# Kernel tuning notes

Hardware: AMD Instinct MI355X
Metric: run time of the kernel (lower is better)

Reference implementation:

```python
import jax, jax.numpy as jnp
import numpy as np

B, N, C, H, KC, STAGES = 8, 4096, 256, 8, 128, 3
C4 = 4 * C
HD = C4 // H
SCALE = (C // H) ** -0.5  # torch uses head_dim of ORIGINAL dim: (256//8)^-0.5


def _l2norm(x, axis):
    # torch: inp / (1e-6 + inp.norm(dim=axis, keepdim=True))
    return x / (1e-6 + jnp.linalg.norm(x, axis=axis, keepdims=True))


def _dta_branch(xc):
    """EM-style clustering on one stream. xc: [B, 4C, N] -> bases [B, 4C, KC]."""
    b, c, n = xc.shape
    # AdaptiveMaxPool1d(KC): N % KC == 0 -> uniform windows of size N//KC
    bases = _l2norm(xc.reshape(b, c, KC, n // KC).max(axis=-1), axis=1)
    xn = xc.transpose(0, 2, 1)  # [B, N, 4C]
    for _ in range(STAGES):
        z = jax.nn.softmax(jnp.einsum('bnc,bck->bnk', xn, bases), axis=2)  # [B,N,KC]
        z = _l2norm(z, axis=1)
        bases = _l2norm(jnp.einsum('bnc,bnk->bck', xn, z), axis=1)  # [B,4C,KC]
    return bases


def setup_inputs() -> dict:
    key = jax.random.key(0)
    ks = jax.random.split(key, 6)
    x = jax.random.normal(ks[0], (B, N, C), jnp.float32)
    Wq = jax.random.normal(ks[1], (C4, C), jnp.float32) * 0.02
    Wk = jax.random.normal(ks[2], (C4, C), jnp.float32) * 0.02
    Wv = jax.random.normal(ks[3], (C4, C), jnp.float32) * 0.02
    Wp = jax.random.normal(ks[4], (C, C4), jnp.float32) * 0.02
    bp = jnp.zeros((C,), jnp.float32)
    return {"x": x, "Wq": Wq, "Wk": Wk, "Wv": Wv, "Wp": Wp, "bp": bp}


def reference(x, Wq, Wk, Wv, Wp, bp):
    # q/k/v projections (bias-free), [B,N,4C]
    q = x @ Wq.T
    k = x @ Wk.T
    v = x @ Wv.T
    # DTA: note torch does `q, k = self.DA(q, k)` where DA(x1,x2) returns
    # (bases_from_x1, bases_from_x2) -> q bases from q-stream, k bases from k-stream.
    qb = _dta_branch(q.transpose(0, 2, 1))  # [B,4C,KC]
    kb = _dta_branch(k.transpose(0, 2, 1))  # [B,4C,KC]
    qh = qb.reshape(B, H, HD, KC)  # == torch q.permute(0,1,3,2): [B,H,hd,KC]
    kh = kb.reshape(B, H, HD, KC)
    vh = v.transpose(0, 2, 1).reshape(B, H, HD, N)  # [B,H,hd,N]
    # att over cluster axis KC -> [B,H,hd,hd]
    att = jax.nn.softmax(jnp.einsum('bhdk,bhek->bhde', qh, kh) * SCALE, axis=-1)
    o = jnp.einsum('bhde,bhen->bhdn', att, vh)  # [B,H,hd,N]
    # rearrange 'b n_h head_dim n -> b n (n_h head_dim)'
    o = o.transpose(0, 3, 1, 2).reshape(B, N, C4)
    return jax.nn.relu(o @ Wp.T + bp)
```

## Files before the change

kernel.cpp:

```cpp
#include <hip/hip_runtime.h>
#include <hip/hip_bf16.h>

#define NSEQ 4096
#define C4   1024
#define SCALE_F 0.17677669529663687f
#define SLC   524288

typedef __attribute__((ext_vector_type(8))) short bf16x8;
typedef __attribute__((ext_vector_type(4))) float f32x4;
typedef __attribute__((ext_vector_type(8))) unsigned short u16x8;
typedef __attribute__((ext_vector_type(4))) unsigned short u16x4;

__device__ __forceinline__ unsigned short f2b(float x){
  union{float f; unsigned u;} v; v.f = x;
  unsigned r = v.u + 0x7fffu + ((v.u>>16)&1u);
  return (unsigned short)(r>>16);
}
__device__ __forceinline__ unsigned mapf(float x){
  unsigned u = __float_as_uint(x);
  return (u & 0x80000000u) ? ~u : (u | 0x80000000u);
}
__device__ __forceinline__ float unmapf(unsigned m){
  unsigned u = (m & 0x80000000u) ? (m ^ 0x80000000u) : ~m;
  return __uint_as_float(u);
}

typedef __attribute__((address_space(1))) void* gas_p;
typedef __attribute__((address_space(3))) void* las_p;
#define GLDS16(gp, lp) __builtin_amdgcn_global_load_lds((gas_p)(gp), (las_p)(lp), 16, 0, 0)

#define WAITVM8() asm volatile("s_waitcnt vmcnt(8)" ::: "memory")
#define WAITVM4() asm volatile("s_waitcnt vmcnt(4)" ::: "memory")
#define WAITVM0() asm volatile("s_waitcnt vmcnt(0)" ::: "memory")
#define WAITLGKM() asm volatile("s_waitcnt lgkmcnt(0)" ::: "memory")
__device__ __forceinline__ void barrier(){
  asm volatile("" ::: "memory");
  __builtin_amdgcn_s_barrier();
  asm volatile("" ::: "memory");
}

__device__ __forceinline__ void stage128x64s(const unsigned short* G, int row0, int ld, int k0,
                                             unsigned short* lds, int tid){
#pragma unroll
  for (int i = 0; i < 4; ++i){
    int cid = i*256 + tid;
    int r = cid >> 3, c8 = cid & 7;
    GLDS16(G + (row0 + r)*ld + k0 + ((c8 ^ (r & 7))*8), lds + cid*8);
  }
}

template<int LD, int NK, int MA, int MB>
__device__ __forceinline__ void mma_tiles(const unsigned short* ldsA, const unsigned short* ldsB,
                                          f32x4 acc[4][4], int wr, int wc, int lane){
  const int rowg = lane & 15, q4 = lane >> 4;
#pragma unroll
  for (int kc = 0; kc < NK; ++kc){
    bf16x8 a[4], b[4];
#pragma unroll
    for (int mf = 0; mf < 4; ++mf){
      int row = wr*64 + mf*16 + rowg;
      int off;
      if constexpr (MA == 1) off = ((kc*4 + q4) ^ (row & 7)) * 8;
      else                   off = kc*32 + q4*8;
      a[mf] = *(const bf16x8*)(ldsA + row*LD + off);
    }
#pragma unroll
    for (int nf = 0; nf < 4; ++nf){
      int col = wc*64 + nf*16 + rowg;
      int off;
      if constexpr (MB == 1)      off = ((kc*4 + q4) ^ (col & 7)) * 8;
      else if constexpr (MB == 2) off = (kc*32 + q4*8) ^ ((((col>>3) ^ col) & 7) << 3);
      else                        off = kc*32 + q4*8;
      b[nf] = *(const bf16x8*)(ldsB + col*LD + off);
    }
#pragma unroll
    for (int mf = 0; mf < 4; ++mf)
#pragma unroll
      for (int nf = 0; nf < 4; ++nf)
        acc[mf][nf] = __builtin_amdgcn_mfma_f32_16x16x32_bf16(a[mf], b[nf], acc[mf][nf], 0, 0, 0);
  }
}

__global__ __launch_bounds__(256) void k_cast(const float* __restrict__ src,
                                              unsigned short* __restrict__ dst, int n){
  int i = (blockIdx.x*256 + threadIdx.x) * 4;
  if (i < n){
    float4 v = *(const float4*)(src + i);
    u16x4 o = { f2b(v.x), f2b(v.y), f2b(v.z), f2b(v.w) };
    *(u16x4*)(dst + i) = o;
  }
}

__global__ __launch_bounds__(256) void k_transpose_w(const float* __restrict__ src,
                                                     unsigned short* __restrict__ dst,
                                                     int dstLd, int colOff){
  int t = blockIdx.x*256 + threadIdx.x;
  int j = t & 255, r = t >> 8;
  dst[j*dstLd + colOff + r] = f2b(src[r*256 + j]);
}

__global__ __launch_bounds__(256) void k_gemm_qk(const unsigned short* __restrict__ xbf,
                                                 const unsigned short* __restrict__ Wcat,
                                                 unsigned* __restrict__ pooled){
  __shared__ __align__(16) unsigned short ldsA[128*64];
  __shared__ __align__(16) unsigned short ldsB[128*64];
  int tid = threadIdx.x, lane = tid & 63, wid = tid >> 6, wr = wid >> 1, wc = wid & 1;
  int m0 = blockIdx.x*128, n0 = blockIdx.y*128;
  f32x4 acc[4][4] = {};
  for (int k0 = 0; k0 < 256; k0 += 64){
    __syncthreads();
    stage128x64s(xbf,  m0, 256, k0, ldsA, tid);
    stage128x64s(Wcat, n0, 256, k0, ldsB, tid);
    __syncthreads();
    mma_tiles<64,2,1,1>(ldsA, ldsB, acc, wr, wc, lane);
  }
  int colg = lane & 15;
  int b = m0 >> 12, kbase = (m0 & 4095) >> 5;
#pragma unroll
  for (int nf = 0; nf < 4; ++nf){
    float wlo = -3e38f, whi = -3e38f;
#pragma unroll
    for (int r = 0; r < 4; ++r){
      wlo = fmaxf(wlo, fmaxf(acc[0][nf][r], acc[1][nf][r]));
      whi = fmaxf(whi, fmaxf(acc[2][nf][r], acc[3][nf][r]));
    }
    wlo = fmaxf(wlo, __shfl_xor(wlo, 16)); wlo = fmaxf(wlo, __shfl_xor(wlo, 32));
    whi = fmaxf(whi, __shfl_xor(whi, 16)); whi = fmaxf(whi, __shfl_xor(whi, 32));
    if (lane < 16){
      int col = n0 + wc*64 + nf*16 + colg;
      int sbp = b + ((col >> 10) << 3);
      int c4 = col & 1023;
      atomicMax(&pooled[(sbp*128 + kbase + wr*2    )*C4 + c4], mapf(wlo));
      atomicMax(&pooled[(sbp*128 + kbase + wr*2 + 1)*C4 + c4], mapf(whi));
    }
  }
}

__global__ __launch_bounds__(256) void k_norm(const float* __restrict__ bRaw,
                                              const unsigned* __restrict__ pooled,
                                              unsigned short* __restrict__ basesT, int S){
  int row = blockIdx.x, tid = threadIdx.x, lane = tid & 63, wid = tid >> 6;
  float4 v;
  if (S == 0){
    uint4 u = *(const uint4*)(pooled + row*C4 + tid*4);
    v.x = unmapf(u.x); v.y = unmapf(u.y); v.z = unmapf(u.z); v.w = unmapf(u.w);
  } else {
    v = *(const float4*)(bRaw + row*C4 + tid*4);
  }
  float ss = v.x*v.x + v.y*v.y + v.z*v.z + v.w*v.w;
  __shared__ float red[5];
#pragma unroll
  for (int o = 32; o; o >>= 1) ss += __shfl_down(ss, o);
  if (lane == 0) red[wid] = ss;
  __syncthreads();
  if (tid == 0) red[4] = 1.f / (1e-6f + sqrtf(red[0] + red[1] + red[2] + red[3]));
  __syncthreads();
  float inv = red[4];
  u16x4 o4 = { f2b(v.x*inv), f2b(v.y*inv), f2b(v.z*inv), f2b(v.w*inv) };
  *(u16x4*)(basesT + row*C4 + tid*4) = o4;
}

__global__ __launch_bounds__(256) void k_pb(const unsigned short* __restrict__ basesT,
                                            const unsigned short* __restrict__ WcatT,
                                            float* __restrict__ part){
  __shared__ __align__(16) unsigned short ldsA[128*64];
  __shared__ __align__(16) unsigned short ldsB[128*64];
  int tid = threadIdx.x, lane = tid & 63, wid = tid >> 6, wr = wid >> 1, wc = wid & 1;
  int n0 = blockIdx.x*128, sb = blockIdx.y, ks = blockIdx.z;
  const unsigned short* A = basesT + sb*(128*C4);
  int off = (sb >= 8) ? 1024 : 0;
  f32x4 acc[4][4] = {};
  for (int t = 0; t < 4; ++t){
    __syncthreads();
    stage128x64s(A,     0,  C4,   ks*256 + t*64, ldsA, tid);
    stage128x64s(WcatT, n0, 2048, off + ks*256 + t*64, ldsB, tid);
    __syncthreads();
    mma_tiles<64,2,1,1>(ldsA, ldsB, acc, wr, wc, lane);
  }
  int colg = lane & 15, rowg = (lane >> 4) * 4;
#pragma unroll
  for (int mf = 0; mf < 4; ++mf)
#pragma unroll
    for (int nf = 0; nf < 4; ++nf)
#pragma unroll
      for (int r = 0; r < 4; ++r)
        part[ks*SLC + (sb*128 + wr*64 + mf*16 + rowg + r)*256 + n0 + wc*64 + nf*16 + colg]
          = acc[mf][nf][r];
}

__global__ __launch_bounds__(256) void k_redgt(const float* __restrict__ src,
                                               unsigned short* __restrict__ dst, int S){
  int i = (blockIdx.x*256 + threadIdx.x) * 4;
  float4 a = {0.f,0.f,0.f,0.f};
  for (int s = 0; s < S; ++s){
    float4 u = *(const float4*)(src + s*SLC + i);
    a.x += u.x; a.y += u.y; a.z += u.z; a.w += u.w;
  }
  u16x4 o = { f2b(a.x), f2b(a.y), f2b(a.z), f2b(a.w) };
  *(u16x4*)(dst + i) = o;
}

__global__ __launch_bounds__(256) void k_gemm_z(const unsigned short* __restrict__ xbf,
                                                const unsigned short* __restrict__ PBT,
                                                unsigned short* __restrict__ zT){
  __shared__ __align__(16) unsigned short smem[32768];
  __shared__ float redb[2][2][128];
  unsigned short* zt = smem;
  int tid = threadIdx.x, lane = tid & 63, wid = tid >> 6, wr = wid >> 1, wc = wid & 1;
  int m0 = blockIdx.x*128, sb = blockIdx.y;
  const unsigned short* A = xbf + (sb & 7)*(NSEQ*256);
  const unsigned short* B = PBT + sb*(128*256);
  f32x4 acc[4][4] = {};
  stage128x64s(A, m0, 256, 0, smem, tid);
  stage128x64s(B, 0,  256, 0, smem + 16384, tid);
  for (int t = 0; t < 4; ++t){
    int cur = t & 1;
    if (t < 3){
      stage128x64s(A, m0, 256, (t+1)*64, smem + (cur^1)*8192, tid);
      stage128x64s(B, 0,  256, (t+1)*64, smem + 16384 + (cur^1)*8192, tid);
      WAITVM8();
    } else WAITVM0();
    barrier();
    mma_tiles<64,2,1,1>(smem + cur*8192, smem + 16384 + cur*8192, acc, wr, wc, lane);
    WAITLGKM();
    barrier();
  }
  int colg = lane & 15, rowg = (lane >> 4) * 4;
  float sm[4][4];
#pragma unroll
  for (int mf = 0; mf < 4; ++mf)
#pragma unroll
    for (int r = 0; r < 4; ++r){
      float m = fmaxf(fmaxf(acc[mf][0][r], acc[mf][1][r]), fmaxf(acc[mf][2][r], acc[mf][3][r]));
#pragma unroll
      for (int o = 1; o < 16; o <<= 1) m = fmaxf(m, __shfl_xor(m, o));
      if (colg == 0) redb[0][wc][wr*64 + mf*16 + rowg + r] = m;
    }
  barrier();
#pragma unroll
  for (int mf = 0; mf < 4; ++mf)
#pragma unroll
    for (int r = 0; r < 4; ++r){
      int idx = wr*64 + mf*16 + rowg + r;
      float m = fmaxf(redb[0][0][idx], redb[0][1][idx]);
      float s = 0.f;
#pragma unroll
      for (int nf = 0; nf < 4; ++nf){
        float e = __expf(acc[mf][nf][r] - m);
        acc[mf][nf][r] = e; s += e;
      }
#pragma unroll
      for (int o = 1; o < 16; o <<= 1) s += __shfl_xor(s, o);
      if (colg == 0) redb[1][wc][idx] = s;
    }
  barrier();
#pragma unroll
  for (int mf = 0; mf < 4; ++mf)
#pragma unroll
    for (int r = 0; r < 4; ++r){
      int idx = wr*64 + mf*16 + rowg + r;
      sm[mf][r] = 1.f / (redb[1][0][idx] + redb[1][1][idx]);
    }
#pragma unroll
  for (int mf = 0; mf < 4; ++mf)
#pragma unroll
    for (int nf = 0; nf < 4; ++nf){
      int k = wc*64 + nf*16 + colg;
      int swz = (k & 7) << 3;
#pragma unroll
      for (int r = 0; r < 4; ++r){
        int n = wr*64 + mf*16 + rowg + r;
        zt[k*128 + (n ^ swz)] = f2b(acc[mf][nf][r] * sm[mf][r]);
      }
    }
  WAITLGKM();
  barrier();
#pragma unroll
  for (int i = 0; i < 8; ++i){
    int cid = i*256 + tid;
    int kk = cid >> 4, j8 = cid & 15;
    int nbase = (j8*8) ^ ((kk & 7) << 3);
    *(uint4*)(zT + sb*(128*NSEQ) + kk*NSEQ + m0 + nbase) = *(const uint4*)(zt + kk*128 + j8*8);
  }
}

__global__ __launch_bounds__(256) void k_gemm_gt(const unsigned short* __restrict__ xbf,
                                                 const unsigned short* __restrict__ zT,
                                                 float* __restrict__ part){
  __shared__ __align__(16) unsigned short ldsA[2][8192];
  __shared__ __align__(16) unsigned short ldsB[2][8192];
  int tid = threadIdx.x, lane = tid & 63, wid = tid >> 6, wr = wid >> 1, wc = wid & 1;
  int c0 = blockIdx.x*128, sb = blockIdx.y, ks = blockIdx.z;
  const unsigned short* xb = xbf + (sb & 7)*(NSEQ*256);
  const unsigned short* Zt = zT + sb*(128*NSEQ);
  int base = ks*512;
  f32x4 acc[4][4] = {};
  u16x8 vB[4];
  int np_[4], c8_[4];
#pragma unroll
  for (int i = 0; i < 4; ++i){
    int cid = i*256 + tid;
    np_[i] = cid >> 4; c8_[i] = cid & 15;
  }
  stage128x64s(Zt, 0, NSEQ, base, ldsA[0], tid);
#pragma unroll
  for (int i = 0; i < 4; ++i)
    vB[i] = *(const u16x8*)(xb + (base + np_[i])*256 + c0 + c8_[i]*8);
  for (int t = 0; t < 8; ++t){
    int cur = t & 1, n0 = base + t*64;
    if (t < 7){
      stage128x64s(Zt, 0, NSEQ, n0 + 64, ldsA[cur^1], tid);
      WAITVM4();
    } else WAITVM0();
#pragma unroll
    for (int i = 0; i < 4; ++i){
#pragma unroll
      for (int j = 0; j < 8; ++j)
        ldsB[cur][(c8_[i]*8 + j)*64 + (np_[i] ^ (((c8_[i] ^ j) & 7) << 3))] = vB[i][j];
    }
    WAITLGKM();
    barrier();
    if (t < 7){
#pragma unroll
      for (int i = 0; i < 4; ++i)
        vB[i] = *(const u16x8*)(xb + (n0 + 64 + np_[i])*256 + c0 + c8_[i]*8);
    }
    mma_tiles<64,2,1,2>(ldsA[cur], ldsB[cur], acc, wr, wc, lane);
    WAITLGKM();
    barrier();
  }
  int colg = lane & 15, rowg = (lane >> 4) * 4;
#pragma unroll
  for (int mf = 0; mf < 4; ++mf)
#pragma unroll
    for (int nf = 0; nf < 4; ++nf)
#pragma unroll
      for (int r = 0; r < 4; ++r)
        part[ks*SLC + (sb*128 + wr*64 + mf*16 + rowg + r)*256 + c0 + wc*64 + nf*16 + colg]
          = acc[mf][nf][r];
}

__global__ __launch_bounds__(256) void k_pbases(const unsigned short* __restrict__ Wcat,
                                                const unsigned short* __restrict__ GTbf,
                                                float* __restrict__ bRaw){
  __shared__ __align__(16) unsigned short ldsA[128*64];
  __shared__ __align__(16) unsigned short ldsB[128*64];
  int tid = threadIdx.x, lane = tid & 63, wid = tid >> 6, wr = wid >> 1, wc = wid & 1;
  int m0 = blockIdx.x*128, sb = blockIdx.y;
  const unsigned short* A = Wcat + ((sb >= 8) ? 1024*256 : 0);
  const unsigned short* B = GTbf + sb*(128*256);
  f32x4 acc[4][4] = {};
  for (int t = 0; t < 4; ++t){
    __syncthreads();
    stage128x64s(A, m0, 256, t*64, ldsA, tid);
    stage128x64s(B, 0,  256, t*64, ldsB, tid);
    __syncthreads();
    mma_tiles<64,2,1,1>(ldsA, ldsB, acc, wr, wc, lane);
  }
  int colg = lane & 15, rowg = (lane >> 4) * 4;
#pragma unroll
  for (int mf = 0; mf < 4; ++mf)
#pragma unroll
    for (int nf = 0; nf < 4; ++nf)
#pragma unroll
      for (int r = 0; r < 4; ++r){
        int c4 = m0 + wr*64 + mf*16 + rowg + r;
        int k  = wc*64 + nf*16 + colg;
        bRaw[(sb*128 + k)*C4 + c4] = acc[mf][nf][r];
      }
}

__global__ __launch_bounds__(256) void k_attn(const unsigned short* __restrict__ basesT,
                                              unsigned short* __restrict__ attT){
  __shared__ __align__(16) char smem[98816];
  unsigned short* Qlt = (unsigned short*)smem;
  unsigned short* Klt = (unsigned short*)(smem + 32768);
  float* scores       = (float*)smem;
  unsigned short* at  = (unsigned short*)(smem + 66048);
  int tid = threadIdx.x, lane = tid & 63, wid = tid >> 6, wr = wid >> 1, wc = wid & 1;
  int b = blockIdx.x >> 3, h = blockIdx.x & 7;
  const unsigned short* Q = basesT + b*(128*C4) + h*128;
  const unsigned short* K = basesT + (8 + b)*(128*C4) + h*128;
#pragma unroll
  for (int i = 0; i < 8; ++i){
    int cid = i*256 + tid, kk = cid >> 4, c8 = cid & 15;
    u16x8 vq = *(const u16x8*)(Q + kk*C4 + c8*8);
    u16x8 vk = *(const u16x8*)(K + kk*C4 + c8*8);
#pragma unroll
    for (int j = 0; j < 8; ++j){
      Qlt[(c8*8 + j)*128 + kk] = vq[j];
      Klt[(c8*8 + j)*128 + kk] = vk[j];
    }
  }
  __syncthreads();
  f32x4 acc[4][4] = {};
  mma_tiles<128,4,0,0>(Qlt, Klt, acc, wr, wc, lane);
  __syncthreads();
  int colg = lane & 15, rowg = (lane >> 4) * 4;
#pragma unroll
  for (int mf = 0; mf < 4; ++mf)
#pragma unroll
    for (int nf = 0; nf < 4; ++nf)
#pragma unroll
      for (int r = 0; r < 4; ++r)
        scores[(wr*64 + mf*16 + rowg + r)*129 + wc*64 + nf*16 + colg] = acc[mf][nf][r] * SCALE_F;
  __syncthreads();
  if (tid < 128){
    float mx = -3e38f;
    for (int j = 0; j < 128; ++j) mx = fmaxf(mx, scores[tid*129 + j]);
    float s = 0.f;
    for (int j = 0; j < 128; ++j){ float e = __expf(scores[tid*129 + j] - mx); scores[tid*129 + j] = e; s += e; }
    float inv = 1.f / s;
    for (int j = 0; j < 128; ++j) at[j*128 + tid] = f2b(scores[tid*129 + j] * inv);
  }
  __syncthreads();
#pragma unroll
  for (int i = 0; i < 8; ++i){
    int cid = i*256 + tid;
    *(uint4*)(attT + blockIdx.x*16384 + cid*8) = *(const uint4*)(at + cid*8);
  }
}

__global__ __launch_bounds__(256) void k_wpeff(const unsigned short* __restrict__ Wpbf,
                                               const unsigned short* __restrict__ attT,
                                               unsigned short* __restrict__ WpEff){
  __shared__ __align__(16) unsigned short ldsA[128*64];
  __shared__ __align__(16) unsigned short ldsB[128*64];
  int tid = threadIdx.x, lane = tid & 63, wid = tid >> 6, wr = wid >> 1, wc = wid & 1;
  int m0 = blockIdx.x*128;
  int bh = blockIdx.y, b = bh >> 3, h = bh & 7;
  const unsigned short* At = attT + bh*16384;
  f32x4 acc[4][4] = {};
  for (int k0 = 0; k0 < 128; k0 += 64){
    __syncthreads();
    stage128x64s(Wpbf, m0, C4, h*128 + k0, ldsA, tid);
    stage128x64s(At,   0,  128, k0, ldsB, tid);
    __syncthreads();
    mma_tiles<64,2,1,1>(ldsA, ldsB, acc, wr, wc, lane);
  }
  int colg = lane & 15, rowg = (lane >> 4) * 4;
#pragma unroll
  for (int mf = 0; mf < 4; ++mf)
#pragma unroll
    for (int nf = 0; nf < 4; ++nf)
#pragma unroll
      for (int r = 0; r < 4; ++r){
        int row = m0 + wr*64 + mf*16 + rowg + r;
        int col = wc*64 + nf*16 + colg;
        WpEff[b*(256*C4) + row*C4 + h*128 + col] = f2b(acc[mf][nf][r]);
      }
}

__global__ __launch_bounds__(256) void k_gemm_w2(const unsigned short* __restrict__ WpEff,
                                                 const unsigned short* __restrict__ WvT,
                                                 unsigned short* __restrict__ W2){
  __shared__ __align__(16) unsigned short ldsA[128*64];
  __shared__ __align__(16) unsigned short ldsB[128*64];
  int tid = threadIdx.x, lane = tid & 63, wid = tid >> 6, wr = wid >> 1, wc = wid & 1;
  int m0 = blockIdx.x*128, n0 = blockIdx.y*128, b = blockIdx.z;
  const unsigned short* A = WpEff + b*(256*C4);
  f32x4 acc[4][4] = {};
  for (int k0 = 0; k0 < C4; k0 += 64){
    __syncthreads();
    stage128x64s(A,   m0, C4, k0, ldsA, tid);
    stage128x64s(WvT, n0, C4, k0, ldsB, tid);
    __syncthreads();
    mma_tiles<64,2,1,1>(ldsA, ldsB, acc, wr, wc, lane);
  }
  int colg = lane & 15, rowg = (lane >> 4) * 4;
#pragma unroll
  for (int mf = 0; mf < 4; ++mf)
#pragma unroll
    for (int nf = 0; nf < 4; ++nf)
#pragma unroll
      for (int r = 0; r < 4; ++r){
        int row = m0 + wr*64 + mf*16 + rowg + r;
        int col = n0 + wc*64 + nf*16 + colg;
        W2[b*65536 + row*256 + col] = f2b(acc[mf][nf][r]);
      }
}

__global__ __launch_bounds__(256) void k_gemm_out(const unsigned short* __restrict__ xbf,
                                                  const unsigned short* __restrict__ W2,
                                                  const float* __restrict__ bp,
                                                  float* __restrict__ out){
  __shared__ __align__(16) unsigned short ldsA[2][8192];
  __shared__ __align__(16) unsigned short ldsB[2][8192];
  int tid = threadIdx.x, lane = tid & 63, wid = tid >> 6, wr = wid >> 1, wc = wid & 1;
  int m0 = blockIdx.x*128, n0 = blockIdx.y*128, b = blockIdx.z;
  const unsigned short* A = xbf + b*(NSEQ*256);
  const unsigned short* Bm = W2 + b*65536;
  f32x4 acc[4][4] = {};
  stage128x64s(A,  m0, 256, 0, ldsA[0], tid);
  stage128x64s(Bm, n0, 256, 0, ldsB[0], tid);
  for (int t = 0; t < 4; ++t){
    int cur = t & 1;
    if (t < 3){
      stage128x64s(A,  m0, 256, (t+1)*64, ldsA[cur^1], tid);
      stage128x64s(Bm, n0, 256, (t+1)*64, ldsB[cur^1], tid);
      WAITVM8();
    } else WAITVM0();
    barrier();
    mma_tiles<64,2,1,1>(ldsA[cur], ldsB[cur], acc, wr, wc, lane);
    WAITLGKM();
    barrier();
  }
  int colg = lane & 15, rowg = (lane >> 4) * 4;
#pragma unroll
  for (int mf = 0; mf < 4; ++mf)
#pragma unroll
    for (int nf = 0; nf < 4; ++nf){
      int col = n0 + wc*64 + nf*16 + colg;
      float bias = bp[col];
#pragma unroll
      for (int r = 0; r < 4; ++r){
        int row = m0 + wr*64 + mf*16 + rowg + r;
        out[(b*NSEQ + row)*256 + col] = fmaxf(acc[mf][nf][r] + bias, 0.f);
      }
    }
}

extern "C" void kernel_launch(void* const* d_in, const int* in_sizes, int n_in,
                              void* d_out, int out_size, void* d_ws, size_t ws_size,
                              hipStream_t stream){
  (void)in_sizes; (void)n_in; (void)out_size; (void)ws_size;
  const float* x  = (const float*)d_in[0];
  const float* Wq = (const float*)d_in[1];
  const float* Wk = (const float*)d_in[2];
  const float* Wv = (const float*)d_in[3];
  const float* Wp = (const float*)d_in[4];
  const float* bp = (const float*)d_in[5];
  float* out = (float*)d_out;
  char* ws = (char*)d_ws;

  unsigned short* xbf    = (unsigned short*)(ws + 0);
  unsigned short* zT     = (unsigned short*)(ws + 16777216);
  float*          bPart  = (float*)(ws + 50331648);
  float*          bRawP  = (float*)(ws + 67108864);
  unsigned*       pooled = (unsigned*)(ws + 75497472);
  unsigned short* basesT = (unsigned short*)(ws + 83886080);
  unsigned short* PBT    = (unsigned short*)(ws + 88080384);
  unsigned short* GTbf   = (unsigned short*)(ws + 89128960);
  unsigned short* Wcat   = (unsigned short*)(ws + 90177536);
  unsigned short* WcatT  = (unsigned short*)(ws + 91226112);
  unsigned short* WvT    = (unsigned short*)(ws + 92274688);
  unsigned short* Wpbf   = (unsigned short*)(ws + 92798976);
  unsigned short* WpEff  = (unsigned short*)(ws + 93323264);
  unsigned short* attT   = (unsigned short*)(ws + 97517568);
  unsigned short* W2     = (unsigned short*)(ws + 99614720);

  k_cast<<<8192, 256, 0, stream>>>(x,  xbf, 8388608);
  k_cast<<<256,  256, 0, stream>>>(Wq, Wcat,          262144);
  k_cast<<<256,  256, 0, stream>>>(Wk, Wcat + 262144, 262144);
  k_cast<<<256,  256, 0, stream>>>(Wp, Wpbf,          262144);
  k_transpose_w<<<1024, 256, 0, stream>>>(Wv, WvT,   1024, 0);
  k_transpose_w<<<1024, 256, 0, stream>>>(Wq, WcatT, 2048, 0);
  k_transpose_w<<<1024, 256, 0, stream>>>(Wk, WcatT, 2048, 1024);

  (void)hipMemsetAsync(pooled, 0, (size_t)16*128*1024*4, stream);
  k_gemm_qk<<<dim3(256, 16), 256, 0, stream>>>(xbf, Wcat, pooled);
  k_norm<<<2048, 256, 0, stream>>>(bRawP, pooled, basesT, 0);

  for (int st = 0; st < 3; ++st){
    k_pb<<<dim3(2, 16, 4), 256, 0, stream>>>(basesT, WcatT, bPart);
    k_redgt<<<512, 256, 0, stream>>>(bPart, PBT, 4);
    k_gemm_z<<<dim3(32, 16), 256, 0, stream>>>(xbf, PBT, zT);
    k_gemm_gt<<<dim3(2, 16, 8), 256, 0, stream>>>(xbf, zT, bPart);
    k_redgt<<<512, 256, 0, stream>>>(bPart, GTbf, 8);
    k_pbases<<<dim3(8, 16), 256, 0, stream>>>(Wcat, GTbf, bRawP);
    k_norm<<<2048, 256, 0, stream>>>(bRawP, pooled, basesT, 1);
  }

  k_attn<<<64, 256, 0, stream>>>(basesT, attT);
  k_wpeff<<<dim3(2, 64), 256, 0, stream>>>(Wpbf, attT, WpEff);
  k_gemm_w2<<<dim3(2, 2, 8), 256, 0, stream>>>(WpEff, WvT, W2);
  k_gemm_out<<<dim3(32, 2, 8), 256, 0, stream>>>(xbf, W2, bp, out);
}
```

Baseline: 303.3 us.

## Fuse z softmax GEMM with GT accumulation and drop split-K reductions

The z computation is merged with the following G^T = z^T x GEMM, so each block reuses its z tile from LDS, transposes the x tile in LDS and atomically accumulates into an fp32 GT buffer. This removes the zT round trip to global memory and the separate split-K GT kernel and reduce. k_pb now runs the full K loop with double buffering instead of split-K plus a reduce. The weight cast and transpose launches are merged into one kernel. In exchange it adds fp32 atomics, a memset per stage, fewer blocks for k_pb, and a non-deterministic summation order.

```diff
diff --git a/kernel.cpp b/kernel.cpp
--- a/kernel.cpp
+++ b/kernel.cpp
@@ -4,7 +4,6 @@
 #define NSEQ 4096
 #define C4   1024
 #define SCALE_F 0.17677669529663687f
-#define SLC   524288
 
 typedef __attribute__((ext_vector_type(8))) short bf16x8;
 typedef __attribute__((ext_vector_type(4))) float f32x4;
@@ -30,7 +29,6 @@
 #define GLDS16(gp, lp) __builtin_amdgcn_global_load_lds((gas_p)(gp), (las_p)(lp), 16, 0, 0)
 
 #define WAITVM8() asm volatile("s_waitcnt vmcnt(8)" ::: "memory")
-#define WAITVM4() asm volatile("s_waitcnt vmcnt(4)" ::: "memory")
 #define WAITVM0() asm volatile("s_waitcnt vmcnt(0)" ::: "memory")
 #define WAITLGKM() asm volatile("s_waitcnt lgkmcnt(0)" ::: "memory")
 __device__ __forceinline__ void barrier(){
@@ -91,12 +89,31 @@
   }
 }
 
-__global__ __launch_bounds__(256) void k_transpose_w(const float* __restrict__ src,
-                                                     unsigned short* __restrict__ dst,
-                                                     int dstLd, int colOff){
+__global__ __launch_bounds__(256) void k_wprep(const float* __restrict__ Wq, const float* __restrict__ Wk,
+                                               const float* __restrict__ Wv, const float* __restrict__ Wp,
+                                               unsigned short* __restrict__ Wcat,
+                                               unsigned short* __restrict__ Wpbf,
+                                               unsigned short* __restrict__ WcatT,
+                                               unsigned short* __restrict__ WvT){
   int t = blockIdx.x*256 + threadIdx.x;
-  int j = t & 255, r = t >> 8;
-  dst[j*dstLd + colOff + r] = f2b(src[r*256 + j]);
+  int s = blockIdx.y;
+  if (s < 3){
+    const float* src = (s == 0) ? Wq : (s == 1) ? Wk : Wp;
+    unsigned short* dst = (s == 0) ? Wcat : (s == 1) ? (Wcat + 262144) : Wpbf;
+    int i = t*4;
+    float4 v = *(const float4*)(src + i);
+    u16x4 o = { f2b(v.x), f2b(v.y), f2b(v.z), f2b(v.w) };
+    *(u16x4*)(dst + i) = o;
+  } else {
+    const float* src = (s == 3) ? Wv : (s == 4) ? Wq : Wk;
+    unsigned short* dst = (s == 3) ? WvT : WcatT;
+    int ld  = (s == 3) ? 1024 : 2048;
+    int off = (s == 5) ? 1024 : 0;
+    int j = t & 255, r0 = (t >> 8) * 4;
+    u16x4 o = { f2b(src[(r0+0)*256 + j]), f2b(src[(r0+1)*256 + j]),
+                f2b(src[(r0+2)*256 + j]), f2b(src[(r0+3)*256 + j]) };
+    *(u16x4*)(dst + j*ld + off + r0) = o;
+  }
 }
 
 __global__ __launch_bounds__(256) void k_gemm_qk(const unsigned short* __restrict__ xbf,
@@ -162,20 +179,27 @@
 
 __global__ __launch_bounds__(256) void k_pb(const unsigned short* __restrict__ basesT,
                                             const unsigned short* __restrict__ WcatT,
-                                            float* __restrict__ part){
-  __shared__ __align__(16) unsigned short ldsA[128*64];
-  __shared__ __align__(16) unsigned short ldsB[128*64];
-  int tid = threadIdx.x, lane = tid & 63, wid = tid >> 6, wr = wid >> 1, wc = wid & 1;
-  int n0 = blockIdx.x*128, sb = blockIdx.y, ks = blockIdx.z;
+                                            unsigned short* __restrict__ PBT){
+  __shared__ __align__(16) unsigned short ldsA[2][8192];
+  __shared__ __align__(16) unsigned short ldsB[2][8192];
+  int tid = threadIdx.x, lane = tid & 63, wid = tid >> 6, wr = wid >> 1, wc = wid & 1;
+  int n0 = blockIdx.x*128, sb = blockIdx.y;
   const unsigned short* A = basesT + sb*(128*C4);
   int off = (sb >= 8) ? 1024 : 0;
   f32x4 acc[4][4] = {};
-  for (int t = 0; t < 4; ++t){
-    __syncthreads();
-    stage128x64s(A,     0,  C4,   ks*256 + t*64, ldsA, tid);
-    stage128x64s(WcatT, n0, 2048, off + ks*256 + t*64, ldsB, tid);
-    __syncthreads();
-    mma_tiles<64,2,1,1>(ldsA, ldsB, acc, wr, wc, lane);
+  stage128x64s(A,     0,  C4,   0, ldsA[0], tid);
+  stage128x64s(WcatT, n0, 2048, off, ldsB[0], tid);
+  for (int t = 0; t < 16; ++t){
+    int cur = t & 1;
+    if (t < 15){
+      stage128x64s(A,     0,  C4,   (t+1)*64, ldsA[cur^1], tid);
+      stage128x64s(WcatT, n0, 2048, off + (t+1)*64, ldsB[cur^1], tid);
+      WAITVM8();
+    } else WAITVM0();
+    barrier();
+    mma_tiles<64,2,1,1>(ldsA[cur], ldsB[cur], acc, wr, wc, lane);
+    WAITLGKM();
+    barrier();
   }
   int colg = lane & 15, rowg = (lane >> 4) * 4;
 #pragma unroll
@@ -184,28 +208,17 @@
     for (int nf = 0; nf < 4; ++nf)
 #pragma unroll
       for (int r = 0; r < 4; ++r)
-        part[ks*SLC + (sb*128 + wr*64 + mf*16 + rowg + r)*256 + n0 + wc*64 + nf*16 + colg]
-          = acc[mf][nf][r];
-}
-
-__global__ __launch_bounds__(256) void k_redgt(const float* __restrict__ src,
-                                               unsigned short* __restrict__ dst, int S){
-  int i = (blockIdx.x*256 + threadIdx.x) * 4;
-  float4 a = {0.f,0.f,0.f,0.f};
-  for (int s = 0; s < S; ++s){
-    float4 u = *(const float4*)(src + s*SLC + i);
-    a.x += u.x; a.y += u.y; a.z += u.z; a.w += u.w;
-  }
-  u16x4 o = { f2b(a.x), f2b(a.y), f2b(a.z), f2b(a.w) };
-  *(u16x4*)(dst + i) = o;
-}
-
-__global__ __launch_bounds__(256) void k_gemm_z(const unsigned short* __restrict__ xbf,
-                                                const unsigned short* __restrict__ PBT,
-                                                unsigned short* __restrict__ zT){
+        PBT[(sb*128 + wr*64 + mf*16 + rowg + r)*256 + n0 + wc*64 + nf*16 + colg]
+          = f2b(acc[mf][nf][r]);
+}
+
+__global__ __launch_bounds__(256) void k_zgt(const unsigned short* __restrict__ xbf,
+                                             const unsigned short* __restrict__ PBT,
+                                             float* __restrict__ GT){
   __shared__ __align__(16) unsigned short smem[32768];
   __shared__ float redb[2][2][128];
   unsigned short* zt = smem;
+  unsigned short* xT = smem + 16384;
   int tid = threadIdx.x, lane = tid & 63, wid = tid >> 6, wr = wid >> 1, wc = wid & 1;
   int m0 = blockIdx.x*128, sb = blockIdx.y;
   const unsigned short* A = xbf + (sb & 7)*(NSEQ*256);
@@ -275,69 +288,45 @@
     }
   WAITLGKM();
   barrier();
-#pragma unroll
-  for (int i = 0; i < 8; ++i){
-    int cid = i*256 + tid;
-    int kk = cid >> 4, j8 = cid & 15;
-    int nbase = (j8*8) ^ ((kk & 7) << 3);
-    *(uint4*)(zT + sb*(128*NSEQ) + kk*NSEQ + m0 + nbase) = *(const uint4*)(zt + kk*128 + j8*8);
-  }
-}
-
-__global__ __launch_bounds__(256) void k_gemm_gt(const unsigned short* __restrict__ xbf,
-                                                 const unsigned short* __restrict__ zT,
-                                                 float* __restrict__ part){
-  __shared__ __align__(16) unsigned short ldsA[2][8192];
-  __shared__ __align__(16) unsigned short ldsB[2][8192];
-  int tid = threadIdx.x, lane = tid & 63, wid = tid >> 6, wr = wid >> 1, wc = wid & 1;
-  int c0 = blockIdx.x*128, sb = blockIdx.y, ks = blockIdx.z;
-  const unsigned short* xb = xbf + (sb & 7)*(NSEQ*256);
-  const unsigned short* Zt = zT + sb*(128*NSEQ);
-  int base = ks*512;
-  f32x4 acc[4][4] = {};
-  u16x8 vB[4];
-  int np_[4], c8_[4];
-#pragma unroll
-  for (int i = 0; i < 4; ++i){
-    int cid = i*256 + tid;
-    np_[i] = cid >> 4; c8_[i] = cid & 15;
-  }
-  stage128x64s(Zt, 0, NSEQ, base, ldsA[0], tid);
-#pragma unroll
-  for (int i = 0; i < 4; ++i)
-    vB[i] = *(const u16x8*)(xb + (base + np_[i])*256 + c0 + c8_[i]*8);
-  for (int t = 0; t < 8; ++t){
-    int cur = t & 1, n0 = base + t*64;
-    if (t < 7){
-      stage128x64s(Zt, 0, NSEQ, n0 + 64, ldsA[cur^1], tid);
-      WAITVM4();
-    } else WAITVM0();
-#pragma unroll
-    for (int i = 0; i < 4; ++i){
+  for (int ch = 0; ch < 2; ++ch){
+    u16x8 v[8];
+    int np_[8], c8_[8];
+#pragma unroll
+    for (int i = 0; i < 8; ++i){
+      int cid = i*256 + tid;
+      np_[i] = cid >> 4; c8_[i] = cid & 15;
+      v[i] = *(const u16x8*)(A + (m0 + np_[i])*256 + ch*128 + c8_[i]*8);
+    }
+#pragma unroll
+    for (int i = 0; i < 8; ++i){
 #pragma unroll
       for (int j = 0; j < 8; ++j)
-        ldsB[cur][(c8_[i]*8 + j)*64 + (np_[i] ^ (((c8_[i] ^ j) & 7) << 3))] = vB[i][j];
+        xT[(c8_[i]*8 + j)*128 + (np_[i] ^ (((c8_[i] ^ j) & 7) << 3))] = v[i][j];
     }
     WAITLGKM();
     barrier();
-    if (t < 7){
-#pragma unroll
-      for (int i = 0; i < 4; ++i)
-        vB[i] = *(const u16x8*)(xb + (n0 + 64 + np_[i])*256 + c0 + c8_[i]*8);
-    }
-    mma_tiles<64,2,1,2>(ldsA[cur], ldsB[cur], acc, wr, wc, lane);
-    WAITLGKM();
-    barrier();
-  }
-  int colg = lane & 15, rowg = (lane >> 4) * 4;
-#pragma unroll
-  for (int mf = 0; mf < 4; ++mf)
-#pragma unroll
-    for (int nf = 0; nf < 4; ++nf)
-#pragma unroll
-      for (int r = 0; r < 4; ++r)
-        part[ks*SLC + (sb*128 + wr*64 + mf*16 + rowg + r)*256 + c0 + wc*64 + nf*16 + colg]
-          = acc[mf][nf][r];
+    f32x4 acc2[4][4] = {};
+    mma_tiles<128,4,1,2>(zt, xT, acc2, wr, wc, lane);
+#pragma unroll
+    for (int mf = 0; mf < 4; ++mf)
+#pragma unroll
+      for (int nf = 0; nf < 4; ++nf)
+#pragma unroll
+        for (int r = 0; r < 4; ++r){
+          int k = wr*64 + mf*16 + rowg + r;
+          int c = ch*128 + wc*64 + nf*16 + colg;
+          atomicAdd(&GT[(sb*128 + k)*256 + c], acc2[mf][nf][r]);
+        }
+    barrier();
+  }
+}
+
+__global__ __launch_bounds__(256) void k_castgt(const float* __restrict__ GT,
+                                                unsigned short* __restrict__ GTbf){
+  int i = (blockIdx.x*256 + threadIdx.x) * 4;
+  float4 a = *(const float4*)(GT + i);
+  u16x4 o = { f2b(a.x), f2b(a.y), f2b(a.z), f2b(a.w) };
+  *(u16x4*)(GTbf + i) = o;
 }
 
 __global__ __launch_bounds__(256) void k_pbases(const unsigned short* __restrict__ Wcat,
@@ -534,39 +523,32 @@
   char* ws = (char*)d_ws;
 
   unsigned short* xbf    = (unsigned short*)(ws + 0);
-  unsigned short* zT     = (unsigned short*)(ws + 16777216);
-  float*          bPart  = (float*)(ws + 50331648);
-  float*          bRawP  = (float*)(ws + 67108864);
-  unsigned*       pooled = (unsigned*)(ws + 75497472);
-  unsigned short* basesT = (unsigned short*)(ws + 83886080);
-  unsigned short* PBT    = (unsigned short*)(ws + 88080384);
-  unsigned short* GTbf   = (unsigned short*)(ws + 89128960);
-  unsigned short* Wcat   = (unsigned short*)(ws + 90177536);
-  unsigned short* WcatT  = (unsigned short*)(ws + 91226112);
-  unsigned short* WvT    = (unsigned short*)(ws + 92274688);
-  unsigned short* Wpbf   = (unsigned short*)(ws + 92798976);
-  unsigned short* WpEff  = (unsigned short*)(ws + 93323264);
-  unsigned short* attT   = (unsigned short*)(ws + 97517568);
-  unsigned short* W2     = (unsigned short*)(ws + 99614720);
-
-  k_cast<<<8192, 256, 0, stream>>>(x,  xbf, 8388608);
-  k_cast<<<256,  256, 0, stream>>>(Wq, Wcat,          262144);
-  k_cast<<<256,  256, 0, stream>>>(Wk, Wcat + 262144, 262144);
-  k_cast<<<256,  256, 0, stream>>>(Wp, Wpbf,          262144);
-  k_transpose_w<<<1024, 256, 0, stream>>>(Wv, WvT,   1024, 0);
-  k_transpose_w<<<1024, 256, 0, stream>>>(Wq, WcatT, 2048, 0);
-  k_transpose_w<<<1024, 256, 0, stream>>>(Wk, WcatT, 2048, 1024);
+  unsigned*       pooled = (unsigned*)(ws + 16777216);
+  float*          bRawP  = (float*)(ws + 25165824);
+  unsigned short* basesT = (unsigned short*)(ws + 33554432);
+  unsigned short* WpEff  = (unsigned short*)(ws + 37748736);
+  unsigned short* attT   = (unsigned short*)(ws + 41943040);
+  float*          GT     = (float*)(ws + 44040192);
+  unsigned short* PBT    = (unsigned short*)(ws + 46137344);
+  unsigned short* GTbf   = (unsigned short*)(ws + 47185920);
+  unsigned short* Wcat   = (unsigned short*)(ws + 48234496);
+  unsigned short* WcatT  = (unsigned short*)(ws + 49283072);
+  unsigned short* W2     = (unsigned short*)(ws + 50331648);
+  unsigned short* WvT    = (unsigned short*)(ws + 51380224);
+  unsigned short* Wpbf   = (unsigned short*)(ws + 51904512);
+
+  k_cast<<<8192, 256, 0, stream>>>(x, xbf, 8388608);
+  k_wprep<<<dim3(256, 6), 256, 0, stream>>>(Wq, Wk, Wv, Wp, Wcat, Wpbf, WcatT, WvT);
 
   (void)hipMemsetAsync(pooled, 0, (size_t)16*128*1024*4, stream);
   k_gemm_qk<<<dim3(256, 16), 256, 0, stream>>>(xbf, Wcat, pooled);
   k_norm<<<2048, 256, 0, stream>>>(bRawP, pooled, basesT, 0);
 
   for (int st = 0; st < 3; ++st){
-    k_pb<<<dim3(2, 16, 4), 256, 0, stream>>>(basesT, WcatT, bPart);
-    k_redgt<<<512, 256, 0, stream>>>(bPart, PBT, 4);
-    k_gemm_z<<<dim3(32, 16), 256, 0, stream>>>(xbf, PBT, zT);
-    k_gemm_gt<<<dim3(2, 16, 8), 256, 0, stream>>>(xbf, zT, bPart);
-    k_redgt<<<512, 256, 0, stream>>>(bPart, GTbf, 8);
+    k_pb<<<dim3(2, 16), 256, 0, stream>>>(basesT, WcatT, PBT);
+    (void)hipMemsetAsync(GT, 0, (size_t)16*128*256*4, stream);
+    k_zgt<<<dim3(32, 16), 256, 0, stream>>>(xbf, PBT, GT);
+    k_castgt<<<512, 256, 0, stream>>>(GT, GTbf);
     k_pbases<<<dim3(8, 16), 256, 0, stream>>>(Wcat, GTbf, bRawP);
     k_norm<<<2048, 256, 0, stream>>>(bRawP, pooled, basesT, 1);
   }
```

New measurement: 410.3 us. 1.35x slower.

## Merge weight prep kernels and drop split-K reduction in k_pb

Applied to the files above, without the earlier changes.

Six weight cast/transpose launches are merged into one k_wprep kernel, and the transpose now writes four bf16 values per thread. k_pb no longer uses split-K: each block loops over the full K=1024 with double-buffered LDS and writes bf16 PBT directly, which removes one k_redgt launch and an fp32 partial round-trip per stage. The trade-off is that k_pb now runs only 32 blocks, so its parallelism is lower. The workspace offsets are also repacked.

```diff
diff --git a/kernel.cpp b/kernel.cpp
--- a/kernel.cpp
+++ b/kernel.cpp
@@ -91,12 +91,31 @@
   }
 }
 
-__global__ __launch_bounds__(256) void k_transpose_w(const float* __restrict__ src,
-                                                     unsigned short* __restrict__ dst,
-                                                     int dstLd, int colOff){
+__global__ __launch_bounds__(256) void k_wprep(const float* __restrict__ Wq, const float* __restrict__ Wk,
+                                               const float* __restrict__ Wv, const float* __restrict__ Wp,
+                                               unsigned short* __restrict__ Wcat,
+                                               unsigned short* __restrict__ Wpbf,
+                                               unsigned short* __restrict__ WcatT,
+                                               unsigned short* __restrict__ WvT){
   int t = blockIdx.x*256 + threadIdx.x;
-  int j = t & 255, r = t >> 8;
-  dst[j*dstLd + colOff + r] = f2b(src[r*256 + j]);
+  int s = blockIdx.y;
+  if (s < 3){
+    const float* src = (s == 0) ? Wq : (s == 1) ? Wk : Wp;
+    unsigned short* dst = (s == 0) ? Wcat : (s == 1) ? (Wcat + 262144) : Wpbf;
+    int i = t*4;
+    float4 v = *(const float4*)(src + i);
+    u16x4 o = { f2b(v.x), f2b(v.y), f2b(v.z), f2b(v.w) };
+    *(u16x4*)(dst + i) = o;
+  } else {
+    const float* src = (s == 3) ? Wv : (s == 4) ? Wq : Wk;
+    unsigned short* dst = (s == 3) ? WvT : WcatT;
+    int ld  = (s == 3) ? 1024 : 2048;
+    int off = (s == 5) ? 1024 : 0;
+    int j = t & 255, r0 = (t >> 8) * 4;
+    u16x4 o = { f2b(src[(r0+0)*256 + j]), f2b(src[(r0+1)*256 + j]),
+                f2b(src[(r0+2)*256 + j]), f2b(src[(r0+3)*256 + j]) };
+    *(u16x4*)(dst + j*ld + off + r0) = o;
+  }
 }
 
 __global__ __launch_bounds__(256) void k_gemm_qk(const unsigned short* __restrict__ xbf,
@@ -162,20 +181,27 @@
 
 __global__ __launch_bounds__(256) void k_pb(const unsigned short* __restrict__ basesT,
                                             const unsigned short* __restrict__ WcatT,
-                                            float* __restrict__ part){
-  __shared__ __align__(16) unsigned short ldsA[128*64];
-  __shared__ __align__(16) unsigned short ldsB[128*64];
-  int tid = threadIdx.x, lane = tid & 63, wid = tid >> 6, wr = wid >> 1, wc = wid & 1;
-  int n0 = blockIdx.x*128, sb = blockIdx.y, ks = blockIdx.z;
+                                            unsigned short* __restrict__ PBT){
+  __shared__ __align__(16) unsigned short ldsA[2][8192];
+  __shared__ __align__(16) unsigned short ldsB[2][8192];
+  int tid = threadIdx.x, lane = tid & 63, wid = tid >> 6, wr = wid >> 1, wc = wid & 1;
+  int n0 = blockIdx.x*128, sb = blockIdx.y;
   const unsigned short* A = basesT + sb*(128*C4);
   int off = (sb >= 8) ? 1024 : 0;
   f32x4 acc[4][4] = {};
-  for (int t = 0; t < 4; ++t){
-    __syncthreads();
-    stage128x64s(A,     0,  C4,   ks*256 + t*64, ldsA, tid);
-    stage128x64s(WcatT, n0, 2048, off + ks*256 + t*64, ldsB, tid);
-    __syncthreads();
-    mma_tiles<64,2,1,1>(ldsA, ldsB, acc, wr, wc, lane);
+  stage128x64s(A,     0,  C4,   0, ldsA[0], tid);
+  stage128x64s(WcatT, n0, 2048, off, ldsB[0], tid);
+  for (int t = 0; t < 16; ++t){
+    int cur = t & 1;
+    if (t < 15){
+      stage128x64s(A,     0,  C4,   (t+1)*64, ldsA[cur^1], tid);
+      stage128x64s(WcatT, n0, 2048, off + (t+1)*64, ldsB[cur^1], tid);
+      WAITVM8();
+    } else WAITVM0();
+    barrier();
+    mma_tiles<64,2,1,1>(ldsA[cur], ldsB[cur], acc, wr, wc, lane);
+    WAITLGKM();
+    barrier();
   }
   int colg = lane & 15, rowg = (lane >> 4) * 4;
 #pragma unroll
@@ -184,20 +210,8 @@
     for (int nf = 0; nf < 4; ++nf)
 #pragma unroll
       for (int r = 0; r < 4; ++r)
-        part[ks*SLC + (sb*128 + wr*64 + mf*16 + rowg + r)*256 + n0 + wc*64 + nf*16 + colg]
-          = acc[mf][nf][r];
-}
-
-__global__ __launch_bounds__(256) void k_redgt(const float* __restrict__ src,
-                                               unsigned short* __restrict__ dst, int S){
-  int i = (blockIdx.x*256 + threadIdx.x) * 4;
-  float4 a = {0.f,0.f,0.f,0.f};
-  for (int s = 0; s < S; ++s){
-    float4 u = *(const float4*)(src + s*SLC + i);
-    a.x += u.x; a.y += u.y; a.z += u.z; a.w += u.w;
-  }
-  u16x4 o = { f2b(a.x), f2b(a.y), f2b(a.z), f2b(a.w) };
-  *(u16x4*)(dst + i) = o;
+        PBT[(sb*128 + wr*64 + mf*16 + rowg + r)*256 + n0 + wc*64 + nf*16 + colg]
+          = f2b(acc[mf][nf][r]);
 }
 
 __global__ __launch_bounds__(256) void k_gemm_z(const unsigned short* __restrict__ xbf,
@@ -338,6 +352,18 @@
       for (int r = 0; r < 4; ++r)
         part[ks*SLC + (sb*128 + wr*64 + mf*16 + rowg + r)*256 + c0 + wc*64 + nf*16 + colg]
           = acc[mf][nf][r];
+}
+
+__global__ __launch_bounds__(256) void k_redgt(const float* __restrict__ src,
+                                               unsigned short* __restrict__ dst, int S){
+  int i = (blockIdx.x*256 + threadIdx.x) * 4;
+  float4 a = {0.f,0.f,0.f,0.f};
+  for (int s = 0; s < S; ++s){
+    float4 u = *(const float4*)(src + s*SLC + i);
+    a.x += u.x; a.y += u.y; a.z += u.z; a.w += u.w;
+  }
+  u16x4 o = { f2b(a.x), f2b(a.y), f2b(a.z), f2b(a.w) };
+  *(u16x4*)(dst + i) = o;
 }
 
 __global__ __launch_bounds__(256) void k_pbases(const unsigned short* __restrict__ Wcat,
@@ -535,35 +561,29 @@
 
   unsigned short* xbf    = (unsigned short*)(ws + 0);
   unsigned short* zT     = (unsigned short*)(ws + 16777216);
-  float*          bPart  = (float*)(ws + 50331648);
-  float*          bRawP  = (float*)(ws + 67108864);
-  unsigned*       pooled = (unsigned*)(ws + 75497472);
-  unsigned short* basesT = (unsigned short*)(ws + 83886080);
-  unsigned short* PBT    = (unsigned short*)(ws + 88080384);
-  unsigned short* GTbf   = (unsigned short*)(ws + 89128960);
-  unsigned short* Wcat   = (unsigned short*)(ws + 90177536);
-  unsigned short* WcatT  = (unsigned short*)(ws + 91226112);
-  unsigned short* WvT    = (unsigned short*)(ws + 92274688);
-  unsigned short* Wpbf   = (unsigned short*)(ws + 92798976);
-  unsigned short* WpEff  = (unsigned short*)(ws + 93323264);
-  unsigned short* attT   = (unsigned short*)(ws + 97517568);
-  unsigned short* W2     = (unsigned short*)(ws + 99614720);
-
-  k_cast<<<8192, 256, 0, stream>>>(x,  xbf, 8388608);
-  k_cast<<<256,  256, 0, stream>>>(Wq, Wcat,          262144);
-  k_cast<<<256,  256, 0, stream>>>(Wk, Wcat + 262144, 262144);
-  k_cast<<<256,  256, 0, stream>>>(Wp, Wpbf,          262144);
-  k_transpose_w<<<1024, 256, 0, stream>>>(Wv, WvT,   1024, 0);
-  k_transpose_w<<<1024, 256, 0, stream>>>(Wq, WcatT, 2048, 0);
-  k_transpose_w<<<1024, 256, 0, stream>>>(Wk, WcatT, 2048, 1024);
+  float*          bPart  = (float*)(ws + 33554432);
+  unsigned*       pooled = (unsigned*)(ws + 50331648);
+  float*          bRawP  = (float*)(ws + 58720256);
+  unsigned short* basesT = (unsigned short*)(ws + 67108864);
+  unsigned short* WpEff  = (unsigned short*)(ws + 71303168);
+  unsigned short* attT   = (unsigned short*)(ws + 75497472);
+  unsigned short* PBT    = (unsigned short*)(ws + 77594624);
+  unsigned short* GTbf   = (unsigned short*)(ws + 78643200);
+  unsigned short* Wcat   = (unsigned short*)(ws + 79691776);
+  unsigned short* WcatT  = (unsigned short*)(ws + 80740352);
+  unsigned short* W2     = (unsigned short*)(ws + 81788928);
+  unsigned short* WvT    = (unsigned short*)(ws + 82837504);
+  unsigned short* Wpbf   = (unsigned short*)(ws + 83361792);
+
+  k_cast<<<8192, 256, 0, stream>>>(x, xbf, 8388608);
+  k_wprep<<<dim3(256, 6), 256, 0, stream>>>(Wq, Wk, Wv, Wp, Wcat, Wpbf, WcatT, WvT);
 
   (void)hipMemsetAsync(pooled, 0, (size_t)16*128*1024*4, stream);
   k_gemm_qk<<<dim3(256, 16), 256, 0, stream>>>(xbf, Wcat, pooled);
   k_norm<<<2048, 256, 0, stream>>>(bRawP, pooled, basesT, 0);
 
   for (int st = 0; st < 3; ++st){
-    k_pb<<<dim3(2, 16, 4), 256, 0, stream>>>(basesT, WcatT, bPart);
-    k_redgt<<<512, 256, 0, stream>>>(bPart, PBT, 4);
+    k_pb<<<dim3(2, 16), 256, 0, stream>>>(basesT, WcatT, PBT);
     k_gemm_z<<<dim3(32, 16), 256, 0, stream>>>(xbf, PBT, zT);
     k_gemm_gt<<<dim3(2, 16, 8), 256, 0, stream>>>(xbf, zT, bPart);
     k_redgt<<<512, 256, 0, stream>>>(bPart, GTbf, 8);
```

Result: slower. 315.5 us (+4.0%).
